# Kernel optimization log

Measured on AMD Instinct MI355X. Metric: run time of the kernel, lower is better.

Reference implementation:

```python
import jax, jax.numpy as jnp
import numpy as np

N_BASIS = 16


def _kan_layer(x, coeffs, centers):
    # x: [b, in], coeffs: [out, in, n], centers: [n]
    mu = jnp.mean(x, axis=0)
    sd = jnp.std(x, axis=0, ddof=1)  # torch.std is unbiased by default
    xn = jnp.clip((x - mu) / (sd + 1e-6), -3.0, 3.0)
    # Gaussian RBF expansion: [b, in, n]
    basis = jnp.exp(-((xn[..., None] - centers) ** 2) / 0.5)
    return jnp.einsum('bin,oin->bo', basis, coeffs)


def setup_inputs() -> dict:
    key = jax.random.key(0)
    ks = jax.random.split(key, 6)
    B, IN, H = 16384, 256, 512
    return {
        'x': jax.random.normal(ks[0], (B, IN), jnp.float32),
        'coeffs1': jax.random.normal(ks[1], (H, IN, N_BASIS), jnp.float32) * 0.1,
        'coeffs2': jax.random.normal(ks[2], (H, H, N_BASIS), jnp.float32) * 0.1,
        'coeffs3': jax.random.normal(ks[3], (1, H, N_BASIS), jnp.float32) * 0.1,
        'skip_w': jax.random.normal(ks[4], (1, IN), jnp.float32) * 0.05,
        'skip_b': jnp.zeros((1,), jnp.float32),
    }


def reference(x, coeffs1, coeffs2, coeffs3, skip_w, skip_b):
    centers = jnp.linspace(-2.0, 2.0, N_BASIS).astype(x.dtype)
    h = jnp.tanh(_kan_layer(x, coeffs1, centers))
    h = jnp.tanh(_kan_layer(h, coeffs2, centers))
    out = _kan_layer(h, coeffs3, centers)[:, 0]  # squeeze(-1)
    skip = (x @ skip_w.T + skip_b)[:, 0]
    return out + skip
```

## Files before the change

### kernel.cpp

```cpp
#include <hip/hip_runtime.h>
#include <cstdint>
#include <cstddef>

typedef __attribute__((ext_vector_type(8))) _Float16 half8;
typedef __attribute__((ext_vector_type(4))) _Float16 half4;
typedef __attribute__((ext_vector_type(2))) __fp16   fp16x2;
typedef __attribute__((ext_vector_type(4))) float    floatx4;

static constexpr int B_ROWS = 16384;
static constexpr int IN_DIM = 256;
static constexpr int H_DIM  = 512;
static constexpr int NB     = 16;

__device__ __forceinline__ float fast_tanh(float x) {
  float ax = fabsf(x);
  float e  = __expf(2.0f * ax);
  float t  = 1.0f - 2.0f / (e + 1.0f);
  return copysignf(t, x);
}

__device__ __forceinline__ void gld16(const void* g, void* l) {
  __builtin_amdgcn_global_load_lds(
      (const __attribute__((address_space(1))) unsigned int*)g,
      (__attribute__((address_space(3))) unsigned int*)l, 16, 0, 0);
}

__global__ __launch_bounds__(256) void prep_k(const float* __restrict__ c1, _Float16* __restrict__ d1, size_t n41,
                                              const float* __restrict__ c2, _Float16* __restrict__ d2, size_t n42,
                                              const float* __restrict__ X,
                                              float* __restrict__ ps, float* __restrict__ ps2) {
  const int bx = blockIdx.x;
  if (bx < 128) {
    int c     = (bx & 3) * 64 + (threadIdx.x & 63);
    int chunk = threadIdx.x >> 6;
    int seg   = bx >> 2;
    int r0    = seg * 512;
    double s = 0.0, s2 = 0.0;
    for (int r = r0 + chunk; r < r0 + 512; r += 4) {
      float v = X[(size_t)r * IN_DIM + c];
      s += v; s2 += (double)v * (double)v;
    }
    __shared__ float Ls[256], Ls2[256];
    Ls[threadIdx.x] = (float)s; Ls2[threadIdx.x] = (float)s2;
    __syncthreads();
    if (chunk == 0) {
      int cl = threadIdx.x;
      float a  = Ls[cl]  + Ls[cl + 64]  + Ls[cl + 128]  + Ls[cl + 192];
      float b  = Ls2[cl] + Ls2[cl + 64] + Ls2[cl + 128] + Ls2[cl + 192];
      ps [(size_t)seg * IN_DIM + c] = a;
      ps2[(size_t)seg * IN_DIM + c] = b;
    }
  } else {
    size_t tot = n41 + n42;
    int nb_blocks = gridDim.x - 128;
    for (size_t i = (size_t)(bx - 128) * 256 + threadIdx.x; i < tot;
         i += (size_t)nb_blocks * 256) {
      const float4* sp; half4* dp; size_t j;
      if (i < n41) { sp = (const float4*)c1; dp = (half4*)d1; j = i; }
      else         { sp = (const float4*)c2; dp = (half4*)d2; j = i - n41; }
      float4 v = sp[j];
      int nb = (int)((j << 2) & 15);
      half4 r;
      float e0 = -2.f + (float)(nb + 0) * (4.f / 15.f);
      float e1 = -2.f + (float)(nb + 1) * (4.f / 15.f);
      float e2 = -2.f + (float)(nb + 2) * (4.f / 15.f);
      float e3 = -2.f + (float)(nb + 3) * (4.f / 15.f);
      r[0] = (_Float16)(v.x * __expf(-2.f * e0 * e0));
      r[1] = (_Float16)(v.y * __expf(-2.f * e1 * e1));
      r[2] = (_Float16)(v.z * __expf(-2.f * e2 * e2));
      r[3] = (_Float16)(v.w * __expf(-2.f * e3 * e3));
      dp[j] = r;
    }
  }
}

__global__ void stats_final_k(const float* __restrict__ ps,
                              const float* __restrict__ ps2,
                              int segs, int cols, int rows,
                              float* __restrict__ nmi, float* __restrict__ isd) {
  int c = blockIdx.x * blockDim.x + threadIdx.x;
  if (c >= cols) return;
  double s = 0.0, s2 = 0.0;
  for (int g = 0; g < segs; g++) { s += ps[(size_t)g * cols + c]; s2 += ps2[(size_t)g * cols + c]; }
  double mean = s / rows;
  double var  = (s2 - s * s / rows) / (rows - 1);
  if (var < 0.0) var = 0.0;
  float sd = (float)sqrt(var);
  float iv = 1.0f / (sd + 1e-6f);
  isd[c] = iv;
  nmi[c] = -(float)mean * iv;
}

__global__ __launch_bounds__(512, 4) void kan_gemm_fused(const float* __restrict__ X,
                                                         const float* __restrict__ nmi,
                                                         const float* __restrict__ isd,
                                                         const _Float16* __restrict__ Bm,
                                                         float* __restrict__ Hout,
                                                         float* __restrict__ psum,
                                                         float* __restrict__ psum2,
                                                         int C) {
  const int K = C << 4;
  const int steps = K >> 6;
  __shared__ __align__(16) unsigned char LDSB[81920];
  _Float16* const Asb = reinterpret_cast<_Float16*>(LDSB);
  _Float16* const Bsb = reinterpret_cast<_Float16*>(LDSB + 32768);
  const int tid  = threadIdx.x;
  const int w = tid >> 6, lane = tid & 63;
  const int wm = w & 1, wn = (w >> 1) & 1, ksw = w >> 2;
  const int lrow = lane & 15, quad = lane >> 4;
  const int row0 = blockIdx.x * 128;
  const int col0 = blockIdx.y * 128;
  const int kq = ksw * 4 + quad;

  const int s_row = tid >> 3;
  const int s_sl  = tid & 7;
  const int s_seg = s_sl ^ ((s_row >> 1) & 7);
  const _Float16* gB = Bm + (size_t)(col0 + s_row) * K + s_seg * 8;

  const int erow = tid & 127;
  const int eh   = tid >> 7;
  const float* xp  = X   + (size_t)(row0 + erow) * C + eh;
  const float* mup = nmi + eh;
  const float* isp = isd + eh;

  floatx4 acc[4][4] = {};

  auto expand_store = [&](float xr, float ii, float bb, int bufi) {
    float xn = fminf(fmaxf(fmaf(xr, ii, bb), -3.f), 3.f);
    float Wv = __expf(fmaf(-2.f, xn, -8.f) * xn);
    float g  = __expf((16.f / 15.f) * xn);
    float g2 = g * g, g4 = g2 * g2, g8 = g4 * g4;
    fp16x2 gg = __builtin_amdgcn_cvt_pkrtz(g2, g2);
    union { fp16x2 q[4]; half8 v8; } u0, u1;
    u0.q[0] = __builtin_amdgcn_cvt_pkrtz(Wv, Wv * g);
    u0.q[1] = u0.q[0] * gg;
    u0.q[2] = u0.q[1] * gg;
    u0.q[3] = u0.q[2] * gg;
    float W8 = Wv * g8;
    u1.q[0] = __builtin_amdgcn_cvt_pkrtz(W8, W8 * g);
    u1.q[1] = u1.q[0] * gg;
    u1.q[2] = u1.q[1] * gg;
    u1.q[3] = u1.q[2] * gg;
    int ks0 = 2 * eh;
    *(half8*)&Asb[(size_t)bufi * 8192 + (size_t)(ks0 * 128 + erow) * 8]       = u0.v8;
    *(half8*)&Asb[(size_t)bufi * 8192 + (size_t)((ks0 + 1) * 128 + erow) * 8] = u1.v8;
  };

  float x0 = xp[0];
  float a0 = isp[0];
  float b0 = mup[0];
  gld16(gB, &Bsb[(size_t)tid * 8]);
  gld16(gB + (size_t)64 * K, &Bsb[(size_t)(tid + 512) * 8]);
  __builtin_amdgcn_sched_barrier(0);
  gld16(gB + 64, &Bsb[8192 + (size_t)tid * 8]);
  gld16(gB + 64 + (size_t)64 * K, &Bsb[8192 + (size_t)(tid + 512) * 8]);
  __builtin_amdgcn_sched_barrier(0);
  float xv = xp[4];
  float av = isp[4];
  float bv = mup[4];
  expand_store(x0, a0, b0, 0);
  asm volatile("s_waitcnt vmcnt(0)" ::: "memory");
  asm volatile("s_waitcnt lgkmcnt(0)" ::: "memory");
  __builtin_amdgcn_s_barrier();
  __builtin_amdgcn_sched_barrier(0);

  int bcur = 0;
  for (int k = 0; k < steps; k++) {
    const int abuf = k & 1;
    const bool more  = (k + 1 < steps);
    const bool more2 = (k + 2 < steps);
    const int b2 = (bcur == 0) ? 2 : bcur - 1;
    if (more2) {
      gld16(gB + (size_t)(k + 2) * 64, &Bsb[(size_t)b2 * 8192 + (size_t)tid * 8]);
      gld16(gB + (size_t)(k + 2) * 64 + (size_t)64 * K,
            &Bsb[(size_t)b2 * 8192 + (size_t)(tid + 512) * 8]);
      __builtin_amdgcn_sched_barrier(0);
    }
    half8 af[4], bf[4];
#pragma unroll
    for (int t = 0; t < 4; t++) {
      int arow = wm * 64 + t * 16 + lrow;
      af[t] = *(const half8*)&Asb[(size_t)abuf * 8192 + (size_t)(kq * 128 + arow) * 8];
    }
#pragma unroll
    for (int t = 0; t < 4; t++) {
      int brow = wn * 64 + t * 16 + lrow;
      int bchunk = brow * 8 + (kq ^ ((brow >> 1) & 7));
      bf[t] = *(const half8*)&Bsb[(size_t)bcur * 8192 + (size_t)bchunk * 8];
    }
    __builtin_amdgcn_s_setprio(1);
#pragma unroll
    for (int tm = 0; tm < 2; tm++)
#pragma unroll
      for (int tn = 0; tn < 4; tn++)
        acc[tm][tn] = __builtin_amdgcn_mfma_f32_16x16x32_f16(af[tm], bf[tn], acc[tm][tn], 0, 0, 0);
    __builtin_amdgcn_s_setprio(0);
    if (more) {
      expand_store(xv, av, bv, abuf ^ 1);
      if (more2) {
        xv = xp[4 * (k + 2)];
        av = isp[4 * (k + 2)];
        bv = mup[4 * (k + 2)];
      }
    }
    __builtin_amdgcn_s_setprio(1);
#pragma unroll
    for (int tm = 2; tm < 4; tm++)
#pragma unroll
      for (int tn = 0; tn < 4; tn++)
        acc[tm][tn] = __builtin_amdgcn_mfma_f32_16x16x32_f16(af[tm], bf[tn], acc[tm][tn], 0, 0, 0);
    __builtin_amdgcn_s_setprio(0);
    asm volatile("s_waitcnt lgkmcnt(0)" ::: "memory");
    __builtin_amdgcn_s_barrier();
    __builtin_amdgcn_sched_barrier(0);
    bcur = (bcur == 2) ? 0 : bcur + 1;
  }

  float* MB = reinterpret_cast<float*>(LDSB);
  const int p = wm * 2 + wn;
  asm volatile("s_waitcnt vmcnt(0)" ::: "memory");
  if (ksw == 1) {
    float* dst = MB + (size_t)p * 4096;
#pragma unroll
    for (int tm = 0; tm < 4; tm++)
#pragma unroll
      for (int tn = 0; tn < 4; tn++)
        *(floatx4*)&dst[((tm * 4 + tn) * 64 + lane) * 4] = acc[tm][tn];
  }
  asm volatile("s_waitcnt lgkmcnt(0)" ::: "memory");
  __builtin_amdgcn_s_barrier();
  __builtin_amdgcn_sched_barrier(0);

  float* Rs1 = MB + 16384;
  float* Rs2 = Rs1 + 256;
  if (ksw == 0) {
    const float* src = MB + (size_t)p * 4096;
    float s1[4] = {0.f, 0.f, 0.f, 0.f}, s2v[4] = {0.f, 0.f, 0.f, 0.f};
#pragma unroll
    for (int tm = 0; tm < 4; tm++) {
#pragma unroll
      for (int tn = 0; tn < 4; tn++) {
        floatx4 other = *(const floatx4*)&src[((tm * 4 + tn) * 64 + lane) * 4];
        int gcol = col0 + wn * 64 + tn * 16 + lrow;
#pragma unroll
        for (int r = 0; r < 4; r++) {
          int grow = row0 + wm * 64 + tm * 16 + quad * 4 + r;
          float v = fast_tanh(acc[tm][tn][r] + other[r]);
          Hout[(size_t)grow * H_DIM + gcol] = v;
          s1[tn] += v; s2v[tn] += v * v;
        }
      }
    }
#pragma unroll
    for (int tn = 0; tn < 4; tn++) {
      s1[tn]  += __shfl_xor(s1[tn], 16);  s1[tn]  += __shfl_xor(s1[tn], 32);
      s2v[tn] += __shfl_xor(s2v[tn], 16); s2v[tn] += __shfl_xor(s2v[tn], 32);
    }
    if (quad == 0) {
#pragma unroll
      for (int tn = 0; tn < 4; tn++) {
        Rs1[wm * 128 + wn * 64 + tn * 16 + lrow] = s1[tn];
        Rs2[wm * 128 + wn * 64 + tn * 16 + lrow] = s2v[tn];
      }
    }
  }
  asm volatile("s_waitcnt lgkmcnt(0)" ::: "memory");
  __builtin_amdgcn_s_barrier();
  __builtin_amdgcn_sched_barrier(0);
  if (tid < 128) {
    psum [(size_t)blockIdx.x * H_DIM + col0 + tid] = Rs1[tid] + Rs1[128 + tid];
    psum2[(size_t)blockIdx.x * H_DIM + col0 + tid] = Rs2[tid] + Rs2[128 + tid];
  }
}

__global__ __launch_bounds__(256) void layer3_k(const float* __restrict__ H2,
                                                const float* __restrict__ nmi,
                                                const float* __restrict__ isd,
                                                const float* __restrict__ C3,
                                                const float* __restrict__ X,
                                                const float* __restrict__ SW,
                                                const float* __restrict__ SB,
                                                float* __restrict__ OUT) {
  int w = threadIdx.x >> 6, lane = threadIdx.x & 63;
  float Kn[NB];
#pragma unroll
  for (int n = 0; n < NB; n++) {
    float c = -2.f + (float)n * (4.f / 15.f);
    Kn[n] = __expf(-2.f * c * c);
  }
  float sb0 = SB[0];
  int row_base = blockIdx.x * 16 + w * 4;
  for (int r = 0; r < 4; r++) {
    int row = row_base + r;
    float s = 0.f;
#pragma unroll
    for (int j = 0; j < 8; j++) {
      int i = lane + 64 * j;
      float hv = H2[(size_t)row * H_DIM + i];
      float xn = fminf(fmaxf(fmaf(hv, isd[i], nmi[i]), -3.f), 3.f);
      float Wf = __expf(fmaf(-2.f, xn, -8.f) * xn);
      float gf = __expf((16.f / 15.f) * xn);
      const floatx4* cp = (const floatx4*)(C3 + (size_t)i * NB);
      floatx4 c0 = cp[0], c1 = cp[1], c2 = cp[2], c3 = cp[3];
      float p = Wf;
#pragma unroll
      for (int n = 0; n < 4; n++) { s += p * Kn[n]      * c0[n]; p *= gf; }
#pragma unroll
      for (int n = 0; n < 4; n++) { s += p * Kn[n + 4]  * c1[n]; p *= gf; }
#pragma unroll
      for (int n = 0; n < 4; n++) { s += p * Kn[n + 8]  * c2[n]; p *= gf; }
#pragma unroll
      for (int n = 0; n < 4; n++) { s += p * Kn[n + 12] * c3[n]; p *= gf; }
    }
#pragma unroll
    for (int j = 0; j < 4; j++) {
      int i = lane + 64 * j;
      s += X[(size_t)row * IN_DIM + i] * SW[i];
    }
#pragma unroll
    for (int off = 32; off > 0; off >>= 1) s += __shfl_down(s, off);
    if (lane == 0) OUT[row] = s + sb0;
  }
}

extern "C" void kernel_launch(void* const* d_in, const int* in_sizes, int n_in,
                              void* d_out, int out_size, void* d_ws, size_t ws_size,
                              hipStream_t stream) {
  const float* x  = (const float*)d_in[0];
  const float* c1 = (const float*)d_in[1];
  const float* c2 = (const float*)d_in[2];
  const float* c3 = (const float*)d_in[3];
  const float* sw = (const float*)d_in[4];
  const float* sb = (const float*)d_in[5];
  float* out = (float*)d_out;

  const int B = B_ROWS, IN = IN_DIM, H = H_DIM;

  char* ws = (char*)d_ws;
  size_t off = 0;
  auto alloc = [&](size_t bytes) -> void* {
    void* p = ws + off;
    off += (bytes + 255) & ~(size_t)255;
    return p;
  };
  _Float16* C1h = (_Float16*)alloc((size_t)H * IN * NB * 2);
  _Float16* C2h = (_Float16*)alloc((size_t)H * H  * NB * 2);
  float* H1 = (float*)alloc((size_t)B * H * 4);
  float* H2 = (float*)alloc((size_t)B * H * 4);
  float* ps  = (float*)alloc(128 * 512 * 4);
  float* ps2 = (float*)alloc(128 * 512 * 4);
  float* nmi = (float*)alloc(512 * 4);
  float* isd = (float*)alloc(512 * 4);

  prep_k<<<128 + 1024, 256, 0, stream>>>(c1, C1h, (size_t)H * IN * NB / 4,
                                         c2, C2h, (size_t)H * H * NB / 4,
                                         x, ps, ps2);
  stats_final_k<<<1, 256, 0, stream>>>(ps, ps2, 32, IN, B, nmi, isd);

  kan_gemm_fused<<<dim3(B / 128, 4), 512, 0, stream>>>(x, nmi, isd, C1h, H1, ps, ps2, IN);
  stats_final_k<<<2, 256, 0, stream>>>(ps, ps2, 128, H, B, nmi, isd);

  kan_gemm_fused<<<dim3(B / 128, 4), 512, 0, stream>>>(H1, nmi, isd, C2h, H2, ps, ps2, H);
  stats_final_k<<<2, 256, 0, stream>>>(ps, ps2, 128, H, B, nmi, isd);

  layer3_k<<<B / 16, 256, 0, stream>>>(H2, nmi, isd, c3, x, sw, sb, out);
}
```

Baseline: 457.3 us.

## Pack normalization stats into float2 and stagger expand/MFMA order across k-split waves

The per-column scale and shift are packed into one float2 array, so each expand step issues one global load instead of two. In the GEMM main loop the two k-split wave groups now order their work differently. Group 0 keeps the split MFMA, expand, MFMA sequence, while group 1 expands first and then issues all 16 MFMAs. The aim is to spread the expansion ALU work and the MFMA bursts across waves so they overlap better on the SIMDs. The cost is a divergent branch per wave group and possibly different register pressure.

```diff
diff --git a/kernel.cpp b/kernel.cpp
--- a/kernel.cpp
+++ b/kernel.cpp
@@ -77,7 +77,8 @@
 __global__ void stats_final_k(const float* __restrict__ ps,
                               const float* __restrict__ ps2,
                               int segs, int cols, int rows,
-                              float* __restrict__ nmi, float* __restrict__ isd) {
+                              float* __restrict__ nmi, float* __restrict__ isd,
+                              float2* __restrict__ snpk) {
   int c = blockIdx.x * blockDim.x + threadIdx.x;
   if (c >= cols) return;
   double s = 0.0, s2 = 0.0;
@@ -87,13 +88,14 @@
   if (var < 0.0) var = 0.0;
   float sd = (float)sqrt(var);
   float iv = 1.0f / (sd + 1e-6f);
+  float nm = -(float)mean * iv;
   isd[c] = iv;
-  nmi[c] = -(float)mean * iv;
+  nmi[c] = nm;
+  snpk[c] = make_float2(iv, nm);
 }
 
 __global__ __launch_bounds__(512, 4) void kan_gemm_fused(const float* __restrict__ X,
-                                                         const float* __restrict__ nmi,
-                                                         const float* __restrict__ isd,
+                                                         const float2* __restrict__ snpk,
                                                          const _Float16* __restrict__ Bm,
                                                          float* __restrict__ Hout,
                                                          float* __restrict__ psum,
@@ -119,14 +121,13 @@
 
   const int erow = tid & 127;
   const int eh   = tid >> 7;
-  const float* xp  = X   + (size_t)(row0 + erow) * C + eh;
-  const float* mup = nmi + eh;
-  const float* isp = isd + eh;
+  const float*  xp  = X    + (size_t)(row0 + erow) * C + eh;
+  const float2* snp = snpk + eh;
 
   floatx4 acc[4][4] = {};
 
-  auto expand_store = [&](float xr, float ii, float bb, int bufi) {
-    float xn = fminf(fmaxf(fmaf(xr, ii, bb), -3.f), 3.f);
+  auto expand_store = [&](float xr, float2 sn, int bufi) {
+    float xn = fminf(fmaxf(fmaf(xr, sn.x, sn.y), -3.f), 3.f);
     float Wv = __expf(fmaf(-2.f, xn, -8.f) * xn);
     float g  = __expf((16.f / 15.f) * xn);
     float g2 = g * g, g4 = g2 * g2, g8 = g4 * g4;
@@ -146,19 +147,17 @@
     *(half8*)&Asb[(size_t)bufi * 8192 + (size_t)((ks0 + 1) * 128 + erow) * 8] = u1.v8;
   };
 
-  float x0 = xp[0];
-  float a0 = isp[0];
-  float b0 = mup[0];
+  float  x0  = xp[0];
+  float2 sn0 = snp[0];
   gld16(gB, &Bsb[(size_t)tid * 8]);
   gld16(gB + (size_t)64 * K, &Bsb[(size_t)(tid + 512) * 8]);
   __builtin_amdgcn_sched_barrier(0);
   gld16(gB + 64, &Bsb[8192 + (size_t)tid * 8]);
   gld16(gB + 64 + (size_t)64 * K, &Bsb[8192 + (size_t)(tid + 512) * 8]);
   __builtin_amdgcn_sched_barrier(0);
-  float xv = xp[4];
-  float av = isp[4];
-  float bv = mup[4];
-  expand_store(x0, a0, b0, 0);
+  float  xv = xp[4];
+  float2 sv = snp[4];
+  expand_store(x0, sn0, 0);
   asm volatile("s_waitcnt vmcnt(0)" ::: "memory");
   asm volatile("s_waitcnt lgkmcnt(0)" ::: "memory");
   __builtin_amdgcn_s_barrier();
@@ -177,39 +176,56 @@
       __builtin_amdgcn_sched_barrier(0);
     }
     half8 af[4], bf[4];
-#pragma unroll
-    for (int t = 0; t < 4; t++) {
-      int arow = wm * 64 + t * 16 + lrow;
-      af[t] = *(const half8*)&Asb[(size_t)abuf * 8192 + (size_t)(kq * 128 + arow) * 8];
-    }
-#pragma unroll
-    for (int t = 0; t < 4; t++) {
-      int brow = wn * 64 + t * 16 + lrow;
-      int bchunk = brow * 8 + (kq ^ ((brow >> 1) & 7));
-      bf[t] = *(const half8*)&Bsb[(size_t)bcur * 8192 + (size_t)bchunk * 8];
-    }
-    __builtin_amdgcn_s_setprio(1);
-#pragma unroll
-    for (int tm = 0; tm < 2; tm++)
-#pragma unroll
-      for (int tn = 0; tn < 4; tn++)
-        acc[tm][tn] = __builtin_amdgcn_mfma_f32_16x16x32_f16(af[tm], bf[tn], acc[tm][tn], 0, 0, 0);
-    __builtin_amdgcn_s_setprio(0);
-    if (more) {
-      expand_store(xv, av, bv, abuf ^ 1);
-      if (more2) {
-        xv = xp[4 * (k + 2)];
-        av = isp[4 * (k + 2)];
-        bv = mup[4 * (k + 2)];
-      }
-    }
-    __builtin_amdgcn_s_setprio(1);
-#pragma unroll
-    for (int tm = 2; tm < 4; tm++)
-#pragma unroll
-      for (int tn = 0; tn < 4; tn++)
-        acc[tm][tn] = __builtin_amdgcn_mfma_f32_16x16x32_f16(af[tm], bf[tn], acc[tm][tn], 0, 0, 0);
-    __builtin_amdgcn_s_setprio(0);
+    auto read_frags = [&]() {
+#pragma unroll
+      for (int t = 0; t < 4; t++) {
+        int arow = wm * 64 + t * 16 + lrow;
+        af[t] = *(const half8*)&Asb[(size_t)abuf * 8192 + (size_t)(kq * 128 + arow) * 8];
+      }
+#pragma unroll
+      for (int t = 0; t < 4; t++) {
+        int brow = wn * 64 + t * 16 + lrow;
+        int bchunk = brow * 8 + (kq ^ ((brow >> 1) & 7));
+        bf[t] = *(const half8*)&Bsb[(size_t)bcur * 8192 + (size_t)bchunk * 8];
+      }
+    };
+    auto do_expand = [&]() {
+      if (more) {
+        expand_store(xv, sv, abuf ^ 1);
+        if (more2) {
+          xv = xp[4 * (k + 2)];
+          sv = snp[4 * (k + 2)];
+        }
+      }
+    };
+    if (ksw == 0) {
+      read_frags();
+      __builtin_amdgcn_s_setprio(1);
+#pragma unroll
+      for (int tm = 0; tm < 2; tm++)
+#pragma unroll
+        for (int tn = 0; tn < 4; tn++)
+          acc[tm][tn] = __builtin_amdgcn_mfma_f32_16x16x32_f16(af[tm], bf[tn], acc[tm][tn], 0, 0, 0);
+      __builtin_amdgcn_s_setprio(0);
+      do_expand();
+      __builtin_amdgcn_s_setprio(1);
+#pragma unroll
+      for (int tm = 2; tm < 4; tm++)
+#pragma unroll
+        for (int tn = 0; tn < 4; tn++)
+          acc[tm][tn] = __builtin_amdgcn_mfma_f32_16x16x32_f16(af[tm], bf[tn], acc[tm][tn], 0, 0, 0);
+      __builtin_amdgcn_s_setprio(0);
+    } else {
+      do_expand();
+      read_frags();
+      __builtin_amdgcn_s_setprio(1);
+#pragma unroll
+      for (int tm = 0; tm < 4; tm++)
+#pragma unroll
+        for (int tn = 0; tn < 4; tn++)
+          acc[tm][tn] = __builtin_amdgcn_mfma_f32_16x16x32_f16(af[tm], bf[tn], acc[tm][tn], 0, 0, 0);
+      __builtin_amdgcn_s_setprio(0);
+    }
     asm volatile("s_waitcnt lgkmcnt(0)" ::: "memory");
     __builtin_amdgcn_s_barrier();
     __builtin_amdgcn_sched_barrier(0);
@@ -351,17 +367,18 @@
   float* ps2 = (float*)alloc(128 * 512 * 4);
   float* nmi = (float*)alloc(512 * 4);
   float* isd = (float*)alloc(512 * 4);
+  float2* snpk = (float2*)alloc(512 * 8);
 
   prep_k<<<128 + 1024, 256, 0, stream>>>(c1, C1h, (size_t)H * IN * NB / 4,
                                          c2, C2h, (size_t)H * H * NB / 4,
                                          x, ps, ps2);
-  stats_final_k<<<1, 256, 0, stream>>>(ps, ps2, 32, IN, B, nmi, isd);
-
-  kan_gemm_fused<<<dim3(B / 128, 4), 512, 0, stream>>>(x, nmi, isd, C1h, H1, ps, ps2, IN);
-  stats_final_k<<<2, 256, 0, stream>>>(ps, ps2, 128, H, B, nmi, isd);
-
-  kan_gemm_fused<<<dim3(B / 128, 4), 512, 0, stream>>>(H1, nmi, isd, C2h, H2, ps, ps2, H);
-  stats_final_k<<<2, 256, 0, stream>>>(ps, ps2, 128, H, B, nmi, isd);
+  stats_final_k<<<1, 256, 0, stream>>>(ps, ps2, 32, IN, B, nmi, isd, snpk);
+
+  kan_gemm_fused<<<dim3(B / 128, 4), 512, 0, stream>>>(x, snpk, C1h, H1, ps, ps2, IN);
+  stats_final_k<<<2, 256, 0, stream>>>(ps, ps2, 128, H, B, nmi, isd, snpk);
+
+  kan_gemm_fused<<<dim3(B / 128, 4), 512, 0, stream>>>(H1, snpk, C2h, H2, ps, ps2, H);
+  stats_final_k<<<2, 256, 0, stream>>>(ps, ps2, 128, H, B, nmi, isd, snpk);
 
   layer3_k<<<B / 16, 256, 0, stream>>>(H2, nmi, isd, c3, x, sw, sb, out);
 }
```

New measurement: 440.1 us. 1.04x faster.
